# Kernel tuning notes

Measured on AMD Instinct MI355X. Metric: run time of the kernel, lower is better.

The kernel has to match this reference:

```python
import jax, jax.numpy as jnp
import numpy as np

D_MODEL = 1024
H = 16
D_K = D_MODEL // H  # 64
RANK = 5
ALPHA = 1.0


def _lora_linear(x, W, b, dW, dB):
    # merged weight: W + alpha * dB @ dW  (shape [out, in]); F.linear -> x @ W_merged.T + b
    Wm = W + ALPHA * (dB @ dW)
    return x @ Wm.T + b


def setup_inputs() -> dict:
    key = jax.random.key(0)
    ks = jax.random.split(key, 16)
    b_s, nq = 2, 2048
    s = 1.0 / np.sqrt(D_MODEL).astype(np.float32)
    inp = {
        "x": jax.random.normal(ks[0], (b_s, nq, D_MODEL), dtype=jnp.float32),
    }
    names = ["q", "k", "v", "o"]
    i = 1
    for n in names:
        inp[f"{n}_w"] = jax.random.normal(ks[i], (D_MODEL, D_MODEL), dtype=jnp.float32) * s; i += 1
        inp[f"{n}_b"] = jnp.zeros((D_MODEL,), dtype=jnp.float32)
        inp[f"{n}_dw"] = jax.random.normal(ks[i], (RANK, D_MODEL), dtype=jnp.float32) * 0.01; i += 1
        inp[f"{n}_db"] = jax.random.normal(ks[i], (D_MODEL, RANK), dtype=jnp.float32) * 0.01; i += 1
    return inp


def reference(x, q_w, q_b, q_dw, q_db, k_w, k_b, k_dw, k_db,
              v_w, v_b, v_dw, v_db, o_w, o_b, o_dw, o_db):
    b_s, nq, _ = x.shape
    q = _lora_linear(x, q_w, q_b, q_dw, q_db).reshape(b_s, nq, H, D_K)
    k = _lora_linear(x, k_w, k_b, k_dw, k_db).reshape(b_s, nq, H, D_K)
    v = _lora_linear(x, v_w, v_b, v_dw, v_db).reshape(b_s, nq, H, D_K)
    # scores: [b, h, q, k]
    att = jnp.einsum("bqhd,bkhd->bhqk", q, k) / np.sqrt(D_K).astype(np.float32)
    att = jax.nn.softmax(att, axis=-1)
    out = jnp.einsum("bhqk,bkhd->bqhd", att, v).reshape(b_s, nq, H * D_K)
    out = _lora_linear(out, o_w, o_b, o_dw, o_db)
    return out
```

## Files before the change

kernel.cpp:

```cpp
#include <hip/hip_runtime.h>
#include <hip/hip_bf16.h>

#define NQ 2048
#define NB 2

typedef unsigned short u16;
typedef unsigned int u32;
typedef _Float16 f16;
typedef __attribute__((ext_vector_type(8))) _Float16 half8;
typedef __attribute__((ext_vector_type(2))) __fp16 fp16x2;
typedef __attribute__((ext_vector_type(4))) float f32x4;

#define MFMAH(A, B, C) __builtin_amdgcn_mfma_f32_16x16x32_f16(A, B, C, 0, 0, 0)

__device__ __forceinline__ u16 f2h(float x) {
    f16 h = (f16)x;
    return *(u16*)&h;
}
__device__ __forceinline__ u32 pk_h2(float a, float b) {
    union { fp16x2 v; u32 u; } c;
    c.v = __builtin_amdgcn_cvt_pkrtz(a, b);
    return c.u;
}
__device__ __forceinline__ float fexp2(float x) {
#if __has_builtin(__builtin_amdgcn_exp2f)
    return __builtin_amdgcn_exp2f(x);
#else
    return exp2f(x);
#endif
}
__device__ __forceinline__ void glds16(const u16* g, u16* l) {
    typedef const __attribute__((address_space(1))) u16 gu16;
    typedef __attribute__((address_space(3))) u16 lu16;
    __builtin_amdgcn_global_load_lds((gu16*)g, (lu16*)l, 16, 0, 0);
}

#define QSCALE 0.18033688011112042f

__global__ __launch_bounds__(256) void merge_w16(
    const float* __restrict__ w0, const float* __restrict__ dw0, const float* __restrict__ db0,
    const float* __restrict__ w1, const float* __restrict__ dw1, const float* __restrict__ db1,
    const float* __restrict__ w2, const float* __restrict__ dw2, const float* __restrict__ db2,
    const float* __restrict__ w3, const float* __restrict__ dw3, const float* __restrict__ db3,
    u16* __restrict__ Wf) {
    int idx = blockIdx.x * 256 + threadIdx.x;
    int row = idx >> 10, col = idx & 1023;
    int which = row >> 10, lr = row & 1023;
    const float* W  = (which == 0) ? w0  : (which == 1) ? w1  : (which == 2) ? w2  : w3;
    const float* dW = (which == 0) ? dw0 : (which == 1) ? dw1 : (which == 2) ? dw2 : dw3;
    const float* dB = (which == 0) ? db0 : (which == 1) ? db1 : (which == 2) ? db2 : db3;
    float acc = W[lr * 1024 + col];
#pragma unroll
    for (int r = 0; r < 5; ++r) acc += dB[lr * 5 + r] * dW[r * 1024 + col];
    if (which == 0) acc *= QSCALE;
    Wf[idx] = f2h(acc);
}

__global__ __launch_bounds__(256) void bias_pack(
    const float* __restrict__ b0, const float* __restrict__ b1,
    const float* __restrict__ b2, const float* __restrict__ b3,
    float* __restrict__ ball) {
    int t = blockIdx.x * 256 + threadIdx.x;
    int which = t >> 10;
    const float* B = (which == 0) ? b0 : (which == 1) ? b1 : (which == 2) ? b2 : b3;
    float v = B[t & 1023];
    if (which == 0) v *= QSCALE;
    ball[t] = v;
}

__global__ __launch_bounds__(256) void xcast(const float* __restrict__ x,
                                             u16* __restrict__ xf) {
    int i4 = (blockIdx.x * 256 + threadIdx.x) * 4;
    float4 v = *(const float4*)&x[i4];
    *(uint2*)&xf[i4] = make_uint2(pk_h2(v.x, v.y), pk_h2(v.z, v.w));
}

template <int TM>
__global__ __launch_bounds__(256) void gemm_f16(
    const u16* __restrict__ Af, const u16* __restrict__ Bf,
    const float* __restrict__ bias,
    float* __restrict__ Cf, u16* __restrict__ Cb, int ldc,
    u16* __restrict__ VtOut) {
    constexpr int MI = TM / 32;
    __shared__ u16 As[2][TM * 32];
    __shared__ u16 Bs[2][128 * 32];
    const int tid = threadIdx.x;
    const int wid = tid >> 6, lane = tid & 63;
    const int ln = lane & 15, quad = lane >> 4;
    const int bm = blockIdx.y * TM, bn = blockIdx.x * 128;
    const int wm = (wid >> 1) * (TM / 2), wn = (wid & 1) * 64;
    const int lrow = lane >> 2;
    const int lchunk = (lane & 3) * 8;

    f32x4 acc[MI][4];
#pragma unroll
    for (int i = 0; i < MI; ++i)
#pragma unroll
        for (int j = 0; j < 4; ++j) acc[i][j] = (f32x4){0.f, 0.f, 0.f, 0.f};

    for (int k0 = 0; k0 < 1024; k0 += 64) {
#pragma unroll
        for (int hf = 0; hf < 2; ++hf) {
#pragma unroll
            for (int p = 0; p < TM / 64; ++p) {
                int r = p * 64 + wid * 16;
                glds16(&Af[(bm + r + lrow) * 1024 + k0 + hf * 32 + lchunk],
                       &As[hf][r * 32]);
            }
#pragma unroll
            for (int p = 0; p < 2; ++p) {
                int r = p * 64 + wid * 16;
                glds16(&Bf[(bn + r + lrow) * 1024 + k0 + hf * 32 + lchunk],
                       &Bs[hf][r * 32]);
            }
        }
        asm volatile("s_waitcnt vmcnt(0)" ::: "memory");
        __syncthreads();

        half8 a[MI][2], b[4][2];
#pragma unroll
        for (int kc = 0; kc < 2; ++kc) {
#pragma unroll
            for (int j = 0; j < 4; ++j)
                b[j][kc] = *(const half8*)&Bs[kc][(wn + j * 16 + ln) * 32 + quad * 8];
#pragma unroll
            for (int i = 0; i < MI; ++i)
                a[i][kc] = *(const half8*)&As[kc][(wm + i * 16 + ln) * 32 + quad * 8];
        }
#pragma unroll
        for (int i = 0; i < MI; ++i)
#pragma unroll
            for (int j = 0; j < 4; ++j) {
                acc[i][j] = MFMAH(a[i][0], b[j][0], acc[i][j]);
                acc[i][j] = MFMAH(a[i][1], b[j][1], acc[i][j]);
            }
        __syncthreads();
    }

    if (VtOut && bn >= 2048) {
#pragma unroll
        for (int i = 0; i < MI; ++i)
#pragma unroll
            for (int j = 0; j < 4; ++j) {
                int col = bn + wn + j * 16 + ln;
                float bv = bias[col];
                int colV = col - 2048;
                int row0 = bm + wm + i * 16 + quad * 4;
                ushort4 pk = make_ushort4(f2h(acc[i][j][0] + bv), f2h(acc[i][j][1] + bv),
                                          f2h(acc[i][j][2] + bv), f2h(acc[i][j][3] + bv));
                *(ushort4*)&VtOut[colV * 4096 + row0] = pk;
            }
        return;
    }

#pragma unroll
    for (int i = 0; i < MI; ++i)
#pragma unroll
        for (int j = 0; j < 4; ++j) {
            int col = bn + wn + j * 16 + ln;
            float bv = bias[col];
#pragma unroll
            for (int r = 0; r < 4; ++r) {
                int row = bm + wm + i * 16 + quad * 4 + r;
                float v = acc[i][j][r] + bv;
                if (Cb) Cb[row * ldc + col] = f2h(v);
                else    Cf[row * ldc + col] = v;
            }
        }
}

__global__ __launch_bounds__(256) void flash_f16(
    const u16* __restrict__ QKV, const u16* __restrict__ Vt,
    u16* __restrict__ AO) {
    __shared__ u16 Ks[2][64 * 72];
    __shared__ u16 Vs[2][64 * 72];
    __shared__ u16 Ps[4][32 * 64];

    const int tid = threadIdx.x;
    const int wid = tid >> 6, lane = tid & 63;
    const int ln = lane & 15, quad = lane >> 4;
    const int qt = blockIdx.x, h = blockIdx.y, b = blockIdx.z;
    const int rowbase = b * NQ;
    const int col0 = h * 64;
    const int q0 = rowbase + qt * 128 + wid * 32;

    const half8 ones = {(f16)1, (f16)1, (f16)1, (f16)1,
                        (f16)1, (f16)1, (f16)1, (f16)1};

    half8 qf[2][2];
#pragma unroll
    for (int mi = 0; mi < 2; ++mi)
#pragma unroll
        for (int kc = 0; kc < 2; ++kc)
            qf[mi][kc] = *(const half8*)&QKV[(q0 + mi * 16 + ln) * 3072 + col0 +
                                             kc * 32 + quad * 8];

    f32x4 accO[4][2];
    f32x4 accS[2];
#pragma unroll
    for (int mi = 0; mi < 2; ++mi) {
        accS[mi] = (f32x4){0.f, 0.f, 0.f, 0.f};
#pragma unroll
        for (int a = 0; a < 4; ++a) accO[a][mi] = (f32x4){0.f, 0.f, 0.f, 0.f};
    }

    const int srow = tid >> 2;
    const int sc0 = (tid & 3) * 16;
    const int NT = NQ / 64;

    const int swz = ln & 7;

    {
        const u16* kg = QKV + (rowbase + srow) * 3072 + 1024 + col0;
        const u16* vg = Vt + (col0 + srow) * 4096 + rowbase;
        *(uint4*)&Ks[0][srow * 72 + sc0]     = *(const uint4*)&kg[sc0];
        *(uint4*)&Ks[0][srow * 72 + sc0 + 8] = *(const uint4*)&kg[sc0 + 8];
        *(uint4*)&Vs[0][srow * 72 + sc0]     = *(const uint4*)&vg[sc0];
        *(uint4*)&Vs[0][srow * 72 + sc0 + 8] = *(const uint4*)&vg[sc0 + 8];
    }
    __syncthreads();

    for (int kt = 0; kt < NT; ++kt) {
        const int cur = kt & 1;
        uint4 nk0, nk1, nv0, nv1;
        if (kt + 1 < NT) {
            const u16* kg = QKV + (rowbase + (kt + 1) * 64 + srow) * 3072 + 1024 + col0;
            const u16* vg = Vt + (col0 + srow) * 4096 + rowbase + (kt + 1) * 64;
            nk0 = *(const uint4*)&kg[sc0];
            nk1 = *(const uint4*)&kg[sc0 + 8];
            nv0 = *(const uint4*)&vg[sc0];
            nv1 = *(const uint4*)&vg[sc0 + 8];
        }

        f32x4 s[4][2];
#pragma unroll
        for (int a = 0; a < 4; ++a) {
            half8 kf0 = *(const half8*)&Ks[cur][(a * 16 + ln) * 72 + quad * 8];
            half8 kf1 = *(const half8*)&Ks[cur][(a * 16 + ln) * 72 + 32 + quad * 8];
#pragma unroll
            for (int mi = 0; mi < 2; ++mi) {
                f32x4 t = (f32x4){0.f, 0.f, 0.f, 0.f};
                t = MFMAH(kf0, qf[mi][0], t);
                t = MFMAH(kf1, qf[mi][1], t);
                s[a][mi] = t;
            }
        }

#pragma unroll
        for (int mi = 0; mi < 2; ++mi)
#pragma unroll
            for (int a = 0; a < 4; ++a) {
                float p0 = fexp2(s[a][mi][0]), p1 = fexp2(s[a][mi][1]);
                float p2 = fexp2(s[a][mi][2]), p3 = fexp2(s[a][mi][3]);
                uint2 w = make_uint2(pk_h2(p0, p1), pk_h2(p2, p3));
                int chunk = 2 * a + (quad >> 1);
                int addr = (mi * 16 + ln) * 64 + ((chunk ^ swz) << 3) + ((quad & 1) << 2);
                *(uint2*)&Ps[wid][addr] = w;
            }

        asm volatile("s_waitcnt lgkmcnt(0)" ::: "memory");

        half8 pf[2][2];
#pragma unroll
        for (int mi = 0; mi < 2; ++mi)
#pragma unroll
            for (int kc = 0; kc < 2; ++kc) {
                int chunk = kc * 4 + quad;
                pf[mi][kc] = *(const half8*)&Ps[wid][(mi * 16 + ln) * 64 +
                                                     ((chunk ^ swz) << 3)];
                accS[mi] = MFMAH(ones, pf[mi][kc], accS[mi]);
            }

#pragma unroll
        for (int a = 0; a < 4; ++a) {
            half8 vf0 = *(const half8*)&Vs[cur][(a * 16 + ln) * 72 + quad * 8];
            half8 vf1 = *(const half8*)&Vs[cur][(a * 16 + ln) * 72 + 32 + quad * 8];
#pragma unroll
            for (int mi = 0; mi < 2; ++mi) {
                accO[a][mi] = MFMAH(vf0, pf[mi][0], accO[a][mi]);
                accO[a][mi] = MFMAH(vf1, pf[mi][1], accO[a][mi]);
            }
        }

        if (kt + 1 < NT) {
            const int nb = cur ^ 1;
            *(uint4*)&Ks[nb][srow * 72 + sc0]     = nk0;
            *(uint4*)&Ks[nb][srow * 72 + sc0 + 8] = nk1;
            *(uint4*)&Vs[nb][srow * 72 + sc0]     = nv0;
            *(uint4*)&Vs[nb][srow * 72 + sc0 + 8] = nv1;
        }
        __syncthreads();
    }

#pragma unroll
    for (int mi = 0; mi < 2; ++mi) {
        float inv = 1.f / accS[mi][0];
        int q = q0 + mi * 16 + ln;
#pragma unroll
        for (int a = 0; a < 4; ++a) {
            ushort4 pk = make_ushort4(f2h(accO[a][mi][0] * inv),
                                      f2h(accO[a][mi][1] * inv),
                                      f2h(accO[a][mi][2] * inv),
                                      f2h(accO[a][mi][3] * inv));
            *(ushort4*)&AO[q * 1024 + col0 + a * 16 + quad * 4] = pk;
        }
    }
}

extern "C" void kernel_launch(void* const* d_in, const int* in_sizes, int n_in,
                              void* d_out, int out_size, void* d_ws, size_t ws_size,
                              hipStream_t stream) {
    const float* x = (const float*)d_in[0];
    const float* w[4]  = {(const float*)d_in[1],  (const float*)d_in[5],
                          (const float*)d_in[9],  (const float*)d_in[13]};
    const float* bv[4] = {(const float*)d_in[2],  (const float*)d_in[6],
                          (const float*)d_in[10], (const float*)d_in[14]};
    const float* dw[4] = {(const float*)d_in[3],  (const float*)d_in[7],
                          (const float*)d_in[11], (const float*)d_in[15]};
    const float* db[4] = {(const float*)d_in[4],  (const float*)d_in[8],
                          (const float*)d_in[12], (const float*)d_in[16]};

    u16* p = (u16*)d_ws;
    u16* Wf  = p; p += 4096 * 1024;
    u16* xf  = p; p += 4096 * 1024;
    u16* QKV = p; p += 4096 * 3072;
    u16* Vt  = p; p += 1024 * 4096;
    float* ball = (float*)p;
    u16* AO = xf;

    merge_w16<<<16384, 256, 0, stream>>>(w[0], dw[0], db[0], w[1], dw[1], db[1],
                                         w[2], dw[2], db[2], w[3], dw[3], db[3], Wf);
    bias_pack<<<16, 256, 0, stream>>>(bv[0], bv[1], bv[2], bv[3], ball);
    xcast<<<4096, 256, 0, stream>>>(x, xf);

    gemm_f16<128><<<dim3(24, 32), 256, 0, stream>>>(xf, Wf, ball,
                                                    nullptr, QKV, 3072, Vt);

    flash_f16<<<dim3(NQ / 128, 16, NB), 256, 0, stream>>>(QKV, Vt, AO);

    gemm_f16<64><<<dim3(8, 64), 256, 0, stream>>>(AO, Wf + 3072 * 1024,
                                                  ball + 3072, (float*)d_out, nullptr, 1024,
                                                  nullptr);
}
```

Before: 225.7 us.

## Stage flash K/V via direct global-to-LDS loads and pass P through permlane swaps

```diff
diff --git a/kernel.cpp b/kernel.cpp
--- a/kernel.cpp
+++ b/kernel.cpp
@@ -10,6 +10,7 @@
 typedef __attribute__((ext_vector_type(8))) _Float16 half8;
 typedef __attribute__((ext_vector_type(2))) __fp16 fp16x2;
 typedef __attribute__((ext_vector_type(4))) float f32x4;
+typedef __attribute__((ext_vector_type(2))) unsigned int u32x2;
 
 #define MFMAH(A, B, C) __builtin_amdgcn_mfma_f32_16x16x32_f16(A, B, C, 0, 0, 0)
 
@@ -34,6 +35,22 @@
     typedef __attribute__((address_space(3))) u16 lu16;
     __builtin_amdgcn_global_load_lds((gu16*)g, (lu16*)l, 16, 0, 0);
 }
+__device__ __forceinline__ void pl32swap(u32& a, u32& b) {
+#if __has_builtin(__builtin_amdgcn_permlane32_swap)
+    u32x2 r = __builtin_amdgcn_permlane32_swap(a, b, false, false);
+    a = r[0]; b = r[1];
+#else
+    asm volatile("v_permlane32_swap_b32 %0, %1" : "+v"(a), "+v"(b));
+#endif
+}
+__device__ __forceinline__ void pl16swap(u32& a, u32& b) {
+#if __has_builtin(__builtin_amdgcn_permlane16_swap)
+    u32x2 r = __builtin_amdgcn_permlane16_swap(a, b, false, false);
+    a = r[0]; b = r[1];
+#else
+    asm volatile("v_permlane16_swap_b32 %0, %1" : "+v"(a), "+v"(b));
+#endif
+}
 
 #define QSCALE 0.18033688011112042f
 
@@ -43,17 +60,23 @@
     const float* __restrict__ w2, const float* __restrict__ dw2, const float* __restrict__ db2,
     const float* __restrict__ w3, const float* __restrict__ dw3, const float* __restrict__ db3,
     u16* __restrict__ Wf) {
-    int idx = blockIdx.x * 256 + threadIdx.x;
-    int row = idx >> 10, col = idx & 1023;
+    int i4 = (blockIdx.x * 256 + threadIdx.x) * 4;
+    int row = i4 >> 10, col = i4 & 1023;
     int which = row >> 10, lr = row & 1023;
     const float* W  = (which == 0) ? w0  : (which == 1) ? w1  : (which == 2) ? w2  : w3;
     const float* dW = (which == 0) ? dw0 : (which == 1) ? dw1 : (which == 2) ? dw2 : dw3;
     const float* dB = (which == 0) ? db0 : (which == 1) ? db1 : (which == 2) ? db2 : db3;
-    float acc = W[lr * 1024 + col];
-#pragma unroll
-    for (int r = 0; r < 5; ++r) acc += dB[lr * 5 + r] * dW[r * 1024 + col];
-    if (which == 0) acc *= QSCALE;
-    Wf[idx] = f2h(acc);
+    float4 acc = *(const float4*)&W[lr * 1024 + col];
+#pragma unroll
+    for (int r = 0; r < 5; ++r) {
+        float s = dB[lr * 5 + r];
+        float4 w4 = *(const float4*)&dW[r * 1024 + col];
+        acc.x += s * w4.x; acc.y += s * w4.y;
+        acc.z += s * w4.z; acc.w += s * w4.w;
+    }
+    if (which == 0) { acc.x *= QSCALE; acc.y *= QSCALE; acc.z *= QSCALE; acc.w *= QSCALE; }
+    ushort4 o = make_ushort4(f2h(acc.x), f2h(acc.y), f2h(acc.z), f2h(acc.w));
+    *(ushort4*)&Wf[i4] = o;
 }
 
 __global__ __launch_bounds__(256) void bias_pack(
@@ -172,9 +195,8 @@
 __global__ __launch_bounds__(256) void flash_f16(
     const u16* __restrict__ QKV, const u16* __restrict__ Vt,
     u16* __restrict__ AO) {
-    __shared__ u16 Ks[2][64 * 72];
-    __shared__ u16 Vs[2][64 * 72];
-    __shared__ u16 Ps[4][32 * 64];
+    __shared__ u16 Ks[2][2][64 * 32];
+    __shared__ u16 Vs[2][2][64 * 32];
 
     const int tid = threadIdx.x;
     const int wid = tid >> 6, lane = tid & 63;
@@ -183,6 +205,8 @@
     const int rowbase = b * NQ;
     const int col0 = h * 64;
     const int q0 = rowbase + qt * 128 + wid * 32;
+    const int lrow = lane >> 2;
+    const int lchunk = (lane & 3) * 8;
 
     const half8 ones = {(f16)1, (f16)1, (f16)1, (f16)1,
                         (f16)1, (f16)1, (f16)1, (f16)1};
@@ -204,39 +228,34 @@
         for (int a = 0; a < 4; ++a) accO[a][mi] = (f32x4){0.f, 0.f, 0.f, 0.f};
     }
 
-    const int srow = tid >> 2;
-    const int sc0 = (tid & 3) * 16;
     const int NT = NQ / 64;
-
-    const int swz = ln & 7;
-
-    {
-        const u16* kg = QKV + (rowbase + srow) * 3072 + 1024 + col0;
-        const u16* vg = Vt + (col0 + srow) * 4096 + rowbase;
-        *(uint4*)&Ks[0][srow * 72 + sc0]     = *(const uint4*)&kg[sc0];
-        *(uint4*)&Ks[0][srow * 72 + sc0 + 8] = *(const uint4*)&kg[sc0 + 8];
-        *(uint4*)&Vs[0][srow * 72 + sc0]     = *(const uint4*)&vg[sc0];
-        *(uint4*)&Vs[0][srow * 72 + sc0 + 8] = *(const uint4*)&vg[sc0 + 8];
-    }
+    const u16* Kg = QKV + (rowbase + wid * 16 + lrow) * 3072 + 1024 + col0 + lchunk;
+    const u16* Vg = Vt + (col0 + wid * 16 + lrow) * 4096 + rowbase + lchunk;
+
+#define STAGE(kt2, bu)                                         \
+    {                                                          \
+        const u16* kg_ = Kg + (kt2) * (64 * 3072);             \
+        const u16* vg_ = Vg + (kt2) * 64;                      \
+        glds16(kg_,      &Ks[bu][0][wid * 512]);               \
+        glds16(kg_ + 32, &Ks[bu][1][wid * 512]);               \
+        glds16(vg_,      &Vs[bu][0][wid * 512]);               \
+        glds16(vg_ + 32, &Vs[bu][1][wid * 512]);               \
+    }
+
+    STAGE(0, 0);
+    asm volatile("s_waitcnt vmcnt(0)" ::: "memory");
     __syncthreads();
 
+#pragma unroll 2
     for (int kt = 0; kt < NT; ++kt) {
         const int cur = kt & 1;
-        uint4 nk0, nk1, nv0, nv1;
-        if (kt + 1 < NT) {
-            const u16* kg = QKV + (rowbase + (kt + 1) * 64 + srow) * 3072 + 1024 + col0;
-            const u16* vg = Vt + (col0 + srow) * 4096 + rowbase + (kt + 1) * 64;
-            nk0 = *(const uint4*)&kg[sc0];
-            nk1 = *(const uint4*)&kg[sc0 + 8];
-            nv0 = *(const uint4*)&vg[sc0];
-            nv1 = *(const uint4*)&vg[sc0 + 8];
-        }
+        if (kt + 1 < NT) STAGE(kt + 1, cur ^ 1);
 
         f32x4 s[4][2];
 #pragma unroll
         for (int a = 0; a < 4; ++a) {
-            half8 kf0 = *(const half8*)&Ks[cur][(a * 16 + ln) * 72 + quad * 8];
-            half8 kf1 = *(const half8*)&Ks[cur][(a * 16 + ln) * 72 + 32 + quad * 8];
+            half8 kf0 = *(const half8*)&Ks[cur][0][(a * 16 + ln) * 32 + quad * 8];
+            half8 kf1 = *(const half8*)&Ks[cur][1][(a * 16 + ln) * 32 + quad * 8];
 #pragma unroll
             for (int mi = 0; mi < 2; ++mi) {
                 f32x4 t = (f32x4){0.f, 0.f, 0.f, 0.f};
@@ -246,35 +265,29 @@
             }
         }
 
+        half8 pf[2][2];
 #pragma unroll
         for (int mi = 0; mi < 2; ++mi)
 #pragma unroll
-            for (int a = 0; a < 4; ++a) {
-                float p0 = fexp2(s[a][mi][0]), p1 = fexp2(s[a][mi][1]);
-                float p2 = fexp2(s[a][mi][2]), p3 = fexp2(s[a][mi][3]);
-                uint2 w = make_uint2(pk_h2(p0, p1), pk_h2(p2, p3));
-                int chunk = 2 * a + (quad >> 1);
-                int addr = (mi * 16 + ln) * 64 + ((chunk ^ swz) << 3) + ((quad & 1) << 2);
-                *(uint2*)&Ps[wid][addr] = w;
-            }
-
-        asm volatile("s_waitcnt lgkmcnt(0)" ::: "memory");
-
-        half8 pf[2][2];
-#pragma unroll
-        for (int mi = 0; mi < 2; ++mi)
-#pragma unroll
             for (int kc = 0; kc < 2; ++kc) {
-                int chunk = kc * 4 + quad;
-                pf[mi][kc] = *(const half8*)&Ps[wid][(mi * 16 + ln) * 64 +
-                                                     ((chunk ^ swz) << 3)];
+                u32 c0 = pk_h2(fexp2(s[2 * kc][mi][0]), fexp2(s[2 * kc][mi][1]));
+                u32 c1 = pk_h2(fexp2(s[2 * kc][mi][2]), fexp2(s[2 * kc][mi][3]));
+                u32 c2 = pk_h2(fexp2(s[2 * kc + 1][mi][0]), fexp2(s[2 * kc + 1][mi][1]));
+                u32 c3 = pk_h2(fexp2(s[2 * kc + 1][mi][2]), fexp2(s[2 * kc + 1][mi][3]));
+                pl32swap(c0, c2);
+                pl32swap(c1, c3);
+                pl16swap(c0, c2);
+                pl16swap(c1, c3);
+                union { u32 u[4]; half8 h; } pu;
+                pu.u[0] = c0; pu.u[1] = c1; pu.u[2] = c2; pu.u[3] = c3;
+                pf[mi][kc] = pu.h;
                 accS[mi] = MFMAH(ones, pf[mi][kc], accS[mi]);
             }
 
 #pragma unroll
         for (int a = 0; a < 4; ++a) {
-            half8 vf0 = *(const half8*)&Vs[cur][(a * 16 + ln) * 72 + quad * 8];
-            half8 vf1 = *(const half8*)&Vs[cur][(a * 16 + ln) * 72 + 32 + quad * 8];
+            half8 vf0 = *(const half8*)&Vs[cur][0][(a * 16 + ln) * 32 + quad * 8];
+            half8 vf1 = *(const half8*)&Vs[cur][1][(a * 16 + ln) * 32 + quad * 8];
 #pragma unroll
             for (int mi = 0; mi < 2; ++mi) {
                 accO[a][mi] = MFMAH(vf0, pf[mi][0], accO[a][mi]);
@@ -282,15 +295,10 @@
             }
         }
 
-        if (kt + 1 < NT) {
-            const int nb = cur ^ 1;
-            *(uint4*)&Ks[nb][srow * 72 + sc0]     = nk0;
-            *(uint4*)&Ks[nb][srow * 72 + sc0 + 8] = nk1;
-            *(uint4*)&Vs[nb][srow * 72 + sc0]     = nv0;
-            *(uint4*)&Vs[nb][srow * 72 + sc0 + 8] = nv1;
-        }
+        asm volatile("s_waitcnt vmcnt(0)" ::: "memory");
         __syncthreads();
     }
+#undef STAGE
 
 #pragma unroll
     for (int mi = 0; mi < 2; ++mi) {
@@ -328,8 +336,8 @@
     float* ball = (float*)p;
     u16* AO = xf;
 
-    merge_w16<<<16384, 256, 0, stream>>>(w[0], dw[0], db[0], w[1], dw[1], db[1],
-                                         w[2], dw[2], db[2], w[3], dw[3], db[3], Wf);
+    merge_w16<<<4096, 256, 0, stream>>>(w[0], dw[0], db[0], w[1], dw[1], db[1],
+                                        w[2], dw[2], db[2], w[3], dw[3], db[3], Wf);
     bias_pack<<<16, 256, 0, stream>>>(bv[0], bv[1], bv[2], bv[3], ball);
     xcast<<<4096, 256, 0, stream>>>(x, xf);
 
```

Result: no change. 227.8 us (+0.9%).
